# Kernel optimization log

Measured on AMD Instinct MI355X. Metric: run time of the kernel, lower is better.

The kernel has to match this reference:

```python
import jax, jax.numpy as jnp
import numpy as np
import math

EMBED_DIM = 1024
NUM_HEADS = 16
HEAD_DIM = EMBED_DIM // NUM_HEADS
ROPE_BASE = 10000.0


def setup_inputs() -> dict:
    key = jax.random.key(0)
    ks = jax.random.split(key, 11)
    B, S, E = 2, 2048, EMBED_DIM
    s = 1.0 / math.sqrt(E)
    return {
        "query": jax.random.normal(ks[0], (B, S, E), jnp.float32),
        "key": jax.random.normal(ks[1], (B, S, E), jnp.float32),
        "value": jax.random.normal(ks[2], (B, S, E), jnp.float32),
        "Wq": jax.random.normal(ks[3], (E, E), jnp.float32) * s,
        "bq": jnp.zeros((E,), jnp.float32),
        "Wk": jax.random.normal(ks[4], (E, E), jnp.float32) * s,
        "bk": jnp.zeros((E,), jnp.float32),
        "Wv": jax.random.normal(ks[5], (E, E), jnp.float32) * s,
        "bv": jnp.zeros((E,), jnp.float32),
        "Wo": jax.random.normal(ks[6], (E, E), jnp.float32) * s,
        "bo": jnp.zeros((E,), jnp.float32),
    }


def _rope_cache(S, D, dtype):
    inv_freq = 1.0 / (ROPE_BASE ** (jnp.arange(0, D, 2, dtype=jnp.float32) / D))
    t = jnp.arange(S, dtype=jnp.float32)
    freqs = t[:, None] * inv_freq[None, :]  # [S, D/2]
    return jnp.cos(freqs).astype(dtype), jnp.sin(freqs).astype(dtype)


def _apply_rope(x, cos, sin):
    # x: [B, H, S, D]; cos/sin: [S, D/2]
    x_even = x[..., 0::2]
    x_odd = x[..., 1::2]
    rot_even = x_even * cos - x_odd * sin
    rot_odd = x_odd * cos + x_even * sin
    # interleave back: [..., D/2, 2] -> [..., D]
    return jnp.stack([rot_even, rot_odd], axis=-1).reshape(x.shape)


def reference(query, key, value, Wq, bq, Wk, bk, Wv, bv, Wo, bo):
    B, S, E = query.shape
    H, D = NUM_HEADS, HEAD_DIM
    q = (query @ Wq.T + bq).reshape(B, S, H, D).transpose(0, 2, 1, 3)
    k = (key @ Wk.T + bk).reshape(B, S, H, D).transpose(0, 2, 1, 3)
    v = (value @ Wv.T + bv).reshape(B, S, H, D).transpose(0, 2, 1, 3)
    cos, sin = _rope_cache(S, D, q.dtype)
    q = _apply_rope(q, cos, sin)
    k = _apply_rope(k, cos, sin)
    scores = jnp.einsum('bhsd,bhtd->bhst', q, k) / math.sqrt(D)
    attn = jax.nn.softmax(scores, axis=-1)
    out = jnp.einsum('bhst,bhtd->bhsd', attn, v)
    out = out.transpose(0, 2, 1, 3).reshape(B, S, E)
    return out @ Wo.T + bo
```

## Files before the change

### kernel.cpp

```cpp
#include <hip/hip_runtime.h>
#include <math.h>

typedef unsigned short u16;
typedef __bf16 bf16x8 __attribute__((ext_vector_type(8)));
typedef float floatx4 __attribute__((ext_vector_type(4)));
typedef float floatx16 __attribute__((ext_vector_type(16)));

#define MFMA16(a, b, c) __builtin_amdgcn_mfma_f32_16x16x32_bf16((a), (b), (c), 0, 0, 0)
#define MFMA32(a, b, c) __builtin_amdgcn_mfma_f32_32x32x16_bf16((a), (b), (c), 0, 0, 0)

__device__ __forceinline__ float bf2f(u16 u) {
  union { float f; unsigned int i; } v; v.i = ((unsigned int)u) << 16; return v.f;
}
__device__ __forceinline__ u16 f2bf(float f) {
  __bf16 h = (__bf16)f;
  union { __bf16 h; u16 u; } v; v.h = h; return v.u;
}
__device__ __forceinline__ bf16x8 cvt8(float4 a, float4 b) {
  bf16x8 r;
  r[0] = (__bf16)a.x; r[1] = (__bf16)a.y; r[2] = (__bf16)a.z; r[3] = (__bf16)a.w;
  r[4] = (__bf16)b.x; r[5] = (__bf16)b.y; r[6] = (__bf16)b.z; r[7] = (__bf16)b.w;
  return r;
}
__device__ __forceinline__ void gl2lds16(const void* g, void* l) {
  __builtin_amdgcn_global_load_lds(
      (const __attribute__((address_space(1))) unsigned int*)g,
      (__attribute__((address_space(3))) unsigned int*)l, 16, 0, 0);
}

struct GemmArgs {
  const void* A[3];
  const float* W[3];
  const float* bias[3];
  void* C[3];
  int out_mode[3];
};

template <int BM, int ABF16>
__global__ __launch_bounds__(256) void gemm_nt(GemmArgs args) {
  const int N = 1024, K = 1024;

  const int NY = gridDim.y;
  const int lin = blockIdx.x + (blockIdx.y << 3) + blockIdx.z * (NY << 3);
  const int chunk = NY * gridDim.z;
  const int nid = (lin & 7) * chunk + (lin >> 3);
  const int z = nid / (NY << 3);
  const int rem = nid - z * (NY << 3);
  const int m0 = (rem >> 3) * BM, n0 = (rem & 7) * 128;

  const float* W = args.W[z];
  const float* bias = args.bias[z];
  const int out_mode = args.out_mode[z];
  constexpr int MI = BM / 32;

  __shared__ __align__(16) char AsB[2][ABF16 ? BM * 64 : BM * 128];
  __shared__ __align__(16) char BsB[2][128 * 128];

  const int t = threadIdx.x;
  const int wave = t >> 6, lane = t & 63;
  const int lr = lane & 15, quad = lane >> 4;
  const int wm = (wave >> 1) * (BM / 2), wn = (wave & 1) * 64;

  auto stage = [&](int kt, int bi) {
    if constexpr (ABF16) {
      const u16* Ab = (const u16*)args.A[z];
      constexpr int NI = BM / 16;
#pragma unroll
      for (int j = 0; j < (NI + 3) / 4; j++) {
        const int ii = wave + j * 4;
        if (NI >= 4 || ii < NI) {
          const int r0 = ii * 16;
          const int row = r0 + (lane >> 2);
          const int cg = (lane & 3) ^ ((lane >> 2) & 3);
          gl2lds16(Ab + (size_t)(m0 + row) * K + kt + cg * 8, AsB[bi] + r0 * 64 + lane * 16);
        }
      }
    } else {
      const float* Af = (const float*)args.A[z];
#pragma unroll
      for (int j = 0; j < BM / 32; j++) {
        const int r0 = wave * (BM / 4) + j * 8;
        const int row = r0 + (lane >> 3);
        const int cg = (lane & 7) ^ ((lane >> 3) & 7);
        gl2lds16(Af + (size_t)(m0 + row) * K + kt + cg * 4, AsB[bi] + r0 * 128 + lane * 16);
      }
    }
#pragma unroll
    for (int j = 0; j < 4; j++) {
      const int r0 = wave * 32 + j * 8;
      const int row = r0 + (lane >> 3);
      const int cg = (lane & 7) ^ ((lane >> 3) & 7);
      gl2lds16(W + (size_t)(n0 + row) * K + kt + cg * 4, BsB[bi] + r0 * 128 + lane * 16);
    }
  };

  floatx4 acc[MI][4] = {};

  stage(0, 0);
  int buf = 0;
  for (int kt = 0; kt < K; kt += 32) {
    __syncthreads();
    if (kt + 32 < K) stage(kt + 32, buf ^ 1);

    bf16x8 af[MI], bf[4];
#pragma unroll
    for (int i = 0; i < MI; i++) {
      const int row = wm + i * 16 + lr;
      if constexpr (ABF16) {
        const int cp = quad ^ (row & 3);
        af[i] = *reinterpret_cast<const bf16x8*>(AsB[buf] + row * 64 + cp * 16);
      } else {
        const int e = row & 7;
        const float4 c0 = *reinterpret_cast<const float4*>(AsB[buf] + row * 128 + ((2 * quad) ^ e) * 16);
        const float4 c1 = *reinterpret_cast<const float4*>(AsB[buf] + row * 128 + ((2 * quad + 1) ^ e) * 16);
        af[i] = cvt8(c0, c1);
      }
    }
#pragma unroll
    for (int i = 0; i < 4; i++) {
      const int row = wn + i * 16 + lr;
      const int e = row & 7;
      const float4 c0 = *reinterpret_cast<const float4*>(BsB[buf] + row * 128 + ((2 * quad) ^ e) * 16);
      const float4 c1 = *reinterpret_cast<const float4*>(BsB[buf] + row * 128 + ((2 * quad + 1) ^ e) * 16);
      bf[i] = cvt8(c0, c1);
    }
#pragma unroll
    for (int mi = 0; mi < MI; mi++)
#pragma unroll
      for (int nf = 0; nf < 4; nf++)
        acc[mi][nf] = MFMA16(af[mi], bf[nf], acc[mi][nf]);
    buf ^= 1;
  }

#pragma unroll
  for (int nf = 0; nf < 4; nf++) {
    const int col = n0 + wn + nf * 16 + lr;
    const float bv = bias[col];
#pragma unroll
    for (int mi = 0; mi < MI; mi++) {
      const int row0 = m0 + wm + mi * 16 + quad * 4;
      if (out_mode == 0) {
        u16* C = (u16*)args.C[z];
#pragma unroll
        for (int r = 0; r < 4; r++)
          C[(row0 + r) * N + col] = f2bf(acc[mi][nf][r] + bv);
      } else if (out_mode == 1) {
        u16* C = (u16*)args.C[z];
        const int h = col >> 6, d = col & 63;
        const int b = row0 >> 11, s = row0 & 2047;
        ushort4 pk;
        pk.x = f2bf(acc[mi][nf][0] + bv);
        pk.y = f2bf(acc[mi][nf][1] + bv);
        pk.z = f2bf(acc[mi][nf][2] + bv);
        pk.w = f2bf(acc[mi][nf][3] + bv);
        *reinterpret_cast<ushort4*>(&C[((b * 16 + h) * 64 + d) * 2048 + s]) = pk;
      } else {
        float* C = (float*)args.C[z];
#pragma unroll
        for (int r = 0; r < 4; r++)
          C[(row0 + r) * N + col] = acc[mi][nf][r] + bv;
      }
    }
  }
}

__global__ __launch_bounds__(256) void rope_kernel(u16* Q, u16* Kb) {
  const int idx = blockIdx.x * 256 + threadIdx.x;
  const int tensor = idx >> 19;
  const int i = idx & 524287;
  u16* P = tensor ? Kb : Q;
  const int row = i >> 7;
  const int cg = i & 127;
  const int s = row & 2047;
  const int col0 = cg * 8;
  const float scale = tensor ? 1.0f : 0.18033688011112042f;
  union { uint4 u; u16 h[8]; } v;
  v.u = *reinterpret_cast<const uint4*>(&P[row * 1024 + col0]);
  const int j0 = (col0 & 63) >> 1;
#pragma unroll
  for (int p = 0; p < 4; p++) {
    const int j = j0 + p;
    const float inv = exp2f(-(float)j * (13.287712379549449f / 32.0f));
    const float f = (float)s * inv;
    float sn, cs;
    sincosf(f, &sn, &cs);
    const float e = bf2f(v.h[2 * p]), o = bf2f(v.h[2 * p + 1]);
    v.h[2 * p]     = f2bf((e * cs - o * sn) * scale);
    v.h[2 * p + 1] = f2bf((o * cs + e * sn) * scale);
  }
  *reinterpret_cast<uint4*>(&P[row * 1024 + col0]) = v.u;
}

#define MAKE_PB(pp, g, out) do {                                              \
    unsigned int wA, wB, wC, wD;                                              \
    asm("v_cvt_pk_bf16_f32 %0, %1, %2" : "=v"(wA) : "v"((pp)[(g)+0]), "v"((pp)[(g)+1])); \
    asm("v_cvt_pk_bf16_f32 %0, %1, %2" : "=v"(wB) : "v"((pp)[(g)+4]), "v"((pp)[(g)+5])); \
    asm("v_cvt_pk_bf16_f32 %0, %1, %2" : "=v"(wC) : "v"((pp)[(g)+2]), "v"((pp)[(g)+3])); \
    asm("v_cvt_pk_bf16_f32 %0, %1, %2" : "=v"(wD) : "v"((pp)[(g)+6]), "v"((pp)[(g)+7])); \
    asm("v_permlane32_swap_b32 %0, %1" : "+v"(wA), "+v"(wB));                 \
    asm("v_permlane32_swap_b32 %0, %1" : "+v"(wC), "+v"(wD));                 \
    union { unsigned int w[4]; bf16x8 v; } u_;                                \
    u_.w[0] = wA; u_.w[1] = wC; u_.w[2] = wB; u_.w[3] = wD;                   \
    (out) = u_.v;                                                             \
  } while (0)

__global__ __launch_bounds__(256, 2) void attn_kernel(const u16* Q, const u16* K,
                                                      const u16* Vt, u16* O) {
  const int lin = blockIdx.x + (blockIdx.y << 4);
  const int nid = (lin & 7) * 64 + (lin >> 3);
  const int bx = nid & 15, bh = nid >> 4;

  const int b = bh >> 4, h = bh & 15;
  const int t = threadIdx.x;
  const int warp = t >> 6, lane = t & 63;
  const int lq = lane & 31, hi = lane >> 5;

  __shared__ __align__(16) u16 Ks[2][64][64];
  __shared__ __align__(16) u16 Vs[2][64][64];

  const int q0 = bx * 128 + warp * 32;

  const u16* qp = &Q[(size_t)(b * 2048 + q0 + lq) * 1024 + h * 64 + hi * 8];
  bf16x8 qf[4];
#pragma unroll
  for (int s = 0; s < 4; s++) qf[s] = *reinterpret_cast<const bf16x8*>(&qp[s * 16]);

  const u16* kbase = &K[(size_t)b * 2048 * 1024 + h * 64];
  const u16* vbase = &Vt[(size_t)bh * 131072];

  const int srr = lane >> 3;
  const int scg = (lane & 7) ^ srr;

  auto stage = [&](int kt2, int bufi) {
#pragma unroll
    for (int j = 0; j < 2; j++) {
      const int r0 = warp * 16 + j * 8;
      const int row = r0 + srr;
      gl2lds16(kbase + (size_t)(kt2 + row) * 1024 + scg * 8, &Ks[bufi][r0][0]);
      gl2lds16(vbase + (size_t)row * 2048 + kt2 + scg * 8, &Vs[bufi][r0][0]);
    }
  };

  floatx16 o0 = {}, o1 = {};
  float m = -1.0e30f, l = 0.0f;

  stage(0, 0);
  int buf = 0;
  for (int kt = 0; kt < 2048; kt += 64) {
    __syncthreads();
    if (kt + 64 < 2048) stage(kt + 64, buf ^ 1);

    bf16x8 kf[2][4], vf[4][2];
#pragma unroll
    for (int kb = 0; kb < 2; kb++) {
      const int r = kb * 32 + lq;
#pragma unroll
      for (int s = 0; s < 4; s++)
        kf[kb][s] = *reinterpret_cast<const bf16x8*>(&Ks[buf][r][((s * 2 + hi) ^ (r & 7)) * 8]);
    }
#pragma unroll
    for (int d = 0; d < 2; d++) {
      const int r = d * 32 + lq;
#pragma unroll
      for (int ks = 0; ks < 4; ks++)
        vf[ks][d] = *reinterpret_cast<const bf16x8*>(&Vs[buf][r][((ks * 2 + hi) ^ (r & 7)) * 8]);
    }

    floatx16 p0 = {}, p1 = {};
#pragma unroll
    for (int s = 0; s < 4; s++) {
      p0 = MFMA32(kf[0][s], qf[s], p0);
      p1 = MFMA32(kf[1][s], qf[s], p1);
    }

    float mx = p0[0];
#pragma unroll
    for (int r = 1; r < 16; r++) mx = fmaxf(mx, p0[r]);
#pragma unroll
    for (int r = 0; r < 16; r++) mx = fmaxf(mx, p1[r]);
    mx = fmaxf(mx, __shfl_xor(mx, 32, 64));
    if (!__all(mx <= m + 10.0f)) {
      const float mn = fmaxf(m, mx);
      const float al = __builtin_amdgcn_exp2f(m - mn);
      m = mn;
      l *= al;
#pragma unroll
      for (int r = 0; r < 16; r++) { o0[r] *= al; o1[r] *= al; }
    }
    float sum = 0.0f;
#pragma unroll
    for (int r = 0; r < 16; r++) { p0[r] = __builtin_amdgcn_exp2f(p0[r] - m); sum += p0[r]; }
#pragma unroll
    for (int r = 0; r < 16; r++) { p1[r] = __builtin_amdgcn_exp2f(p1[r] - m); sum += p1[r]; }
    l += sum + __shfl_xor(sum, 32, 64);

    bf16x8 pb0, pb1, pb2, pb3;
    MAKE_PB(p0, 0, pb0);
    MAKE_PB(p0, 8, pb1);
    MAKE_PB(p1, 0, pb2);
    MAKE_PB(p1, 8, pb3);

    o0 = MFMA32(vf[0][0], pb0, o0);
    o1 = MFMA32(vf[0][1], pb0, o1);
    o0 = MFMA32(vf[1][0], pb1, o0);
    o1 = MFMA32(vf[1][1], pb1, o1);
    o0 = MFMA32(vf[2][0], pb2, o0);
    o1 = MFMA32(vf[2][1], pb2, o1);
    o0 = MFMA32(vf[3][0], pb3, o0);
    o1 = MFMA32(vf[3][1], pb3, o1);

    buf ^= 1;
  }

  const float rl = 1.0f / l;
  u16* op = &O[(size_t)(b * 2048 + q0 + lq) * 1024 + h * 64 + hi * 4];
#pragma unroll
  for (int rq = 0; rq < 4; rq++) {
    ushort4 s0, s1;
    s0.x = f2bf(o0[4 * rq + 0] * rl); s0.y = f2bf(o0[4 * rq + 1] * rl);
    s0.z = f2bf(o0[4 * rq + 2] * rl); s0.w = f2bf(o0[4 * rq + 3] * rl);
    s1.x = f2bf(o1[4 * rq + 0] * rl); s1.y = f2bf(o1[4 * rq + 1] * rl);
    s1.z = f2bf(o1[4 * rq + 2] * rl); s1.w = f2bf(o1[4 * rq + 3] * rl);
    *reinterpret_cast<ushort4*>(&op[rq * 8]) = s0;
    *reinterpret_cast<ushort4*>(&op[rq * 8 + 32]) = s1;
  }
}

extern "C" void kernel_launch(void* const* d_in, const int* in_sizes, int n_in,
                              void* d_out, int out_size, void* d_ws, size_t ws_size,
                              hipStream_t stream) {
  (void)in_sizes; (void)n_in; (void)out_size; (void)ws_size;
  const float* query = (const float*)d_in[0];
  const float* key   = (const float*)d_in[1];
  const float* value = (const float*)d_in[2];
  const float* Wq = (const float*)d_in[3];
  const float* bq = (const float*)d_in[4];
  const float* Wk = (const float*)d_in[5];
  const float* bk = (const float*)d_in[6];
  const float* Wv = (const float*)d_in[7];
  const float* bv = (const float*)d_in[8];
  const float* Wo = (const float*)d_in[9];
  const float* bo = (const float*)d_in[10];

  u16* Qb = (u16*)d_ws;
  u16* Kb = (u16*)d_out;
  u16* Vt = (u16*)d_out + 4194304;

  GemmArgs g1;
  g1.A[0] = query; g1.W[0] = Wq; g1.bias[0] = bq; g1.C[0] = Qb; g1.out_mode[0] = 0;
  g1.A[1] = key;   g1.W[1] = Wk; g1.bias[1] = bk; g1.C[1] = Kb; g1.out_mode[1] = 0;
  g1.A[2] = value; g1.W[2] = Wv; g1.bias[2] = bv; g1.C[2] = Vt; g1.out_mode[2] = 1;
  gemm_nt<64, 0><<<dim3(8, 64, 3), dim3(256), 0, stream>>>(g1);

  rope_kernel<<<dim3(4096), dim3(256), 0, stream>>>(Qb, Kb);

  attn_kernel<<<dim3(16, 32), dim3(256), 0, stream>>>(Qb, Kb, Vt, Qb);

  GemmArgs g2;
  for (int i = 0; i < 3; i++) {
    g2.A[i] = Qb; g2.W[i] = Wo; g2.bias[i] = bo;
    g2.C[i] = d_out; g2.out_mode[i] = 2;
  }
  gemm_nt<32, 1><<<dim3(8, 128, 1), dim3(256), 0, stream>>>(g2);
}
```

Baseline: 261.9 us.

## Pre-convert weights and activations to bf16 and enlarge GEMM tiles

Adds a conversion kernel that casts the four weight matrices and, when workspace allows, the q/k/v activations to bf16 in workspace. The GEMMs can then stage bf16 tiles directly, which halves global and LDS traffic and drops the per-iteration fp32-to-bf16 conversion. The GEMMs also drop double buffering for a single buffer with two barriers, and the tiles grow (BM 64→128 for the projections, 32→64 for the output GEMM). The cost is extra conversion passes over the inputs, loss of load/compute overlap inside the GEMM, and lower grid parallelism.

```diff
diff --git a/kernel.cpp b/kernel.cpp
--- a/kernel.cpp
+++ b/kernel.cpp
@@ -28,15 +28,25 @@
       (__attribute__((address_space(3))) unsigned int*)l, 16, 0, 0);
 }
 
+struct CvtArgs { const float* src[3]; u16* dst[3]; };
+__global__ __launch_bounds__(256) void cvt_kernel(CvtArgs a) {
+  const float* s = a.src[blockIdx.z];
+  u16* d = a.dst[blockIdx.z];
+  const int i = (blockIdx.x * 256 + threadIdx.x) * 8;
+  const float4 x = *reinterpret_cast<const float4*>(s + i);
+  const float4 y = *reinterpret_cast<const float4*>(s + i + 4);
+  *reinterpret_cast<bf16x8*>(&d[i]) = cvt8(x, y);
+}
+
 struct GemmArgs {
   const void* A[3];
-  const float* W[3];
+  const void* W[3];
   const float* bias[3];
   void* C[3];
   int out_mode[3];
 };
 
-template <int BM, int ABF16>
+template <int BM, int ABF16, int WBF16>
 __global__ __launch_bounds__(256) void gemm_nt(GemmArgs args) {
   const int N = 1024, K = 1024;
 
@@ -48,20 +58,19 @@
   const int rem = nid - z * (NY << 3);
   const int m0 = (rem >> 3) * BM, n0 = (rem & 7) * 128;
 
-  const float* W = args.W[z];
   const float* bias = args.bias[z];
   const int out_mode = args.out_mode[z];
   constexpr int MI = BM / 32;
 
-  __shared__ __align__(16) char AsB[2][ABF16 ? BM * 64 : BM * 128];
-  __shared__ __align__(16) char BsB[2][128 * 128];
+  __shared__ __align__(16) char AsB[ABF16 ? BM * 64 : BM * 128];
+  __shared__ __align__(16) char BsB[WBF16 ? 128 * 64 : 128 * 128];
 
   const int t = threadIdx.x;
   const int wave = t >> 6, lane = t & 63;
   const int lr = lane & 15, quad = lane >> 4;
   const int wm = (wave >> 1) * (BM / 2), wn = (wave & 1) * 64;
 
-  auto stage = [&](int kt, int bi) {
+  auto stage = [&](int kt) {
     if constexpr (ABF16) {
       const u16* Ab = (const u16*)args.A[z];
       constexpr int NI = BM / 16;
@@ -72,7 +81,7 @@
           const int r0 = ii * 16;
           const int row = r0 + (lane >> 2);
           const int cg = (lane & 3) ^ ((lane >> 2) & 3);
-          gl2lds16(Ab + (size_t)(m0 + row) * K + kt + cg * 8, AsB[bi] + r0 * 64 + lane * 16);
+          gl2lds16(Ab + (size_t)(m0 + row) * K + kt + cg * 8, AsB + r0 * 64 + lane * 16);
         }
       }
     } else {
@@ -82,25 +91,36 @@
         const int r0 = wave * (BM / 4) + j * 8;
         const int row = r0 + (lane >> 3);
         const int cg = (lane & 7) ^ ((lane >> 3) & 7);
-        gl2lds16(Af + (size_t)(m0 + row) * K + kt + cg * 4, AsB[bi] + r0 * 128 + lane * 16);
-      }
-    }
-#pragma unroll
-    for (int j = 0; j < 4; j++) {
-      const int r0 = wave * 32 + j * 8;
-      const int row = r0 + (lane >> 3);
-      const int cg = (lane & 7) ^ ((lane >> 3) & 7);
-      gl2lds16(W + (size_t)(n0 + row) * K + kt + cg * 4, BsB[bi] + r0 * 128 + lane * 16);
+        gl2lds16(Af + (size_t)(m0 + row) * K + kt + cg * 4, AsB + r0 * 128 + lane * 16);
+      }
+    }
+    if constexpr (WBF16) {
+      const u16* Wb = (const u16*)args.W[z];
+#pragma unroll
+      for (int j = 0; j < 2; j++) {
+        const int r0 = (wave + j * 4) * 16;
+        const int row = r0 + (lane >> 2);
+        const int cg = (lane & 3) ^ ((lane >> 2) & 3);
+        gl2lds16(Wb + (size_t)(n0 + row) * K + kt + cg * 8, BsB + r0 * 64 + lane * 16);
+      }
+    } else {
+      const float* Wf = (const float*)args.W[z];
+#pragma unroll
+      for (int j = 0; j < 4; j++) {
+        const int r0 = wave * 32 + j * 8;
+        const int row = r0 + (lane >> 3);
+        const int cg = (lane & 7) ^ ((lane >> 3) & 7);
+        gl2lds16(Wf + (size_t)(n0 + row) * K + kt + cg * 4, BsB + r0 * 128 + lane * 16);
+      }
     }
   };
 
   floatx4 acc[MI][4] = {};
 
-  stage(0, 0);
-  int buf = 0;
   for (int kt = 0; kt < K; kt += 32) {
     __syncthreads();
-    if (kt + 32 < K) stage(kt + 32, buf ^ 1);
+    stage(kt);
+    __syncthreads();
 
     bf16x8 af[MI], bf[4];
 #pragma unroll
@@ -108,28 +128,32 @@
       const int row = wm + i * 16 + lr;
       if constexpr (ABF16) {
         const int cp = quad ^ (row & 3);
-        af[i] = *reinterpret_cast<const bf16x8*>(AsB[buf] + row * 64 + cp * 16);
+        af[i] = *reinterpret_cast<const bf16x8*>(AsB + row * 64 + cp * 16);
       } else {
         const int e = row & 7;
-        const float4 c0 = *reinterpret_cast<const float4*>(AsB[buf] + row * 128 + ((2 * quad) ^ e) * 16);
-        const float4 c1 = *reinterpret_cast<const float4*>(AsB[buf] + row * 128 + ((2 * quad + 1) ^ e) * 16);
+        const float4 c0 = *reinterpret_cast<const float4*>(AsB + row * 128 + ((2 * quad) ^ e) * 16);
+        const float4 c1 = *reinterpret_cast<const float4*>(AsB + row * 128 + ((2 * quad + 1) ^ e) * 16);
         af[i] = cvt8(c0, c1);
       }
     }
 #pragma unroll
     for (int i = 0; i < 4; i++) {
       const int row = wn + i * 16 + lr;
-      const int e = row & 7;
-      const float4 c0 = *reinterpret_cast<const float4*>(BsB[buf] + row * 128 + ((2 * quad) ^ e) * 16);
-      const float4 c1 = *reinterpret_cast<const float4*>(BsB[buf] + row * 128 + ((2 * quad + 1) ^ e) * 16);
-      bf[i] = cvt8(c0, c1);
+      if constexpr (WBF16) {
+        const int cp = quad ^ (row & 3);
+        bf[i] = *reinterpret_cast<const bf16x8*>(BsB + row * 64 + cp * 16);
+      } else {
+        const int e = row & 7;
+        const float4 c0 = *reinterpret_cast<const float4*>(BsB + row * 128 + ((2 * quad) ^ e) * 16);
+        const float4 c1 = *reinterpret_cast<const float4*>(BsB + row * 128 + ((2 * quad + 1) ^ e) * 16);
+        bf[i] = cvt8(c0, c1);
+      }
     }
 #pragma unroll
     for (int mi = 0; mi < MI; mi++)
 #pragma unroll
       for (int nf = 0; nf < 4; nf++)
         acc[mi][nf] = MFMA16(af[mi], bf[nf], acc[mi][nf]);
-    buf ^= 1;
   }
 
 #pragma unroll
@@ -329,7 +353,7 @@
 extern "C" void kernel_launch(void* const* d_in, const int* in_sizes, int n_in,
                               void* d_out, int out_size, void* d_ws, size_t ws_size,
                               hipStream_t stream) {
-  (void)in_sizes; (void)n_in; (void)out_size; (void)ws_size;
+  (void)in_sizes; (void)n_in; (void)out_size;
   const float* query = (const float*)d_in[0];
   const float* key   = (const float*)d_in[1];
   const float* value = (const float*)d_in[2];
@@ -346,11 +370,51 @@
   u16* Kb = (u16*)d_out;
   u16* Vt = (u16*)d_out + 4194304;
 
+  const bool haveW = ws_size >= (size_t)(8388608 + 4 * 2097152);
+  const bool haveA = ws_size >= (size_t)(8388608 + 4 * 2097152 + 25165824);
+  u16* Wbf = (u16*)d_ws + 4194304;
+  u16* Abf = (u16*)d_ws + 4194304 + 4194304;
+
+  if (haveW) {
+    CvtArgs cw;
+    cw.src[0] = Wq; cw.dst[0] = Wbf;
+    cw.src[1] = Wk; cw.dst[1] = Wbf + 1048576;
+    cw.src[2] = Wv; cw.dst[2] = Wbf + 2097152;
+    cvt_kernel<<<dim3(512, 1, 3), dim3(256), 0, stream>>>(cw);
+    CvtArgs co;
+    co.src[0] = Wo; co.dst[0] = Wbf + 3145728;
+    co.src[1] = Wo; co.dst[1] = Wbf + 3145728;
+    co.src[2] = Wo; co.dst[2] = Wbf + 3145728;
+    cvt_kernel<<<dim3(512, 1, 1), dim3(256), 0, stream>>>(co);
+  }
+  if (haveA) {
+    CvtArgs ca;
+    ca.src[0] = query; ca.dst[0] = Abf;
+    ca.src[1] = key;   ca.dst[1] = Abf + 4194304;
+    ca.src[2] = value; ca.dst[2] = Abf + 8388608;
+    cvt_kernel<<<dim3(2048, 1, 3), dim3(256), 0, stream>>>(ca);
+  }
+
   GemmArgs g1;
-  g1.A[0] = query; g1.W[0] = Wq; g1.bias[0] = bq; g1.C[0] = Qb; g1.out_mode[0] = 0;
-  g1.A[1] = key;   g1.W[1] = Wk; g1.bias[1] = bk; g1.C[1] = Kb; g1.out_mode[1] = 0;
-  g1.A[2] = value; g1.W[2] = Wv; g1.bias[2] = bv; g1.C[2] = Vt; g1.out_mode[2] = 1;
-  gemm_nt<64, 0><<<dim3(8, 64, 3), dim3(256), 0, stream>>>(g1);
+  g1.bias[0] = bq; g1.C[0] = Qb; g1.out_mode[0] = 0;
+  g1.bias[1] = bk; g1.C[1] = Kb; g1.out_mode[1] = 0;
+  g1.bias[2] = bv; g1.C[2] = Vt; g1.out_mode[2] = 1;
+  if (haveA) {
+    g1.A[0] = Abf; g1.A[1] = Abf + 4194304; g1.A[2] = Abf + 8388608;
+  } else {
+    g1.A[0] = query; g1.A[1] = key; g1.A[2] = value;
+  }
+  if (haveW) {
+    g1.W[0] = Wbf; g1.W[1] = Wbf + 1048576; g1.W[2] = Wbf + 2097152;
+  } else {
+    g1.W[0] = Wq; g1.W[1] = Wk; g1.W[2] = Wv;
+  }
+  if (haveA && haveW)
+    gemm_nt<128, 1, 1><<<dim3(8, 32, 3), dim3(256), 0, stream>>>(g1);
+  else if (haveW)
+    gemm_nt<128, 0, 1><<<dim3(8, 32, 3), dim3(256), 0, stream>>>(g1);
+  else
+    gemm_nt<128, 0, 0><<<dim3(8, 32, 3), dim3(256), 0, stream>>>(g1);
 
   rope_kernel<<<dim3(4096), dim3(256), 0, stream>>>(Qb, Kb);
 
@@ -358,8 +422,12 @@
 
   GemmArgs g2;
   for (int i = 0; i < 3; i++) {
-    g2.A[i] = Qb; g2.W[i] = Wo; g2.bias[i] = bo;
+    g2.A[i] = Qb; g2.bias[i] = bo;
     g2.C[i] = d_out; g2.out_mode[i] = 2;
-  }
-  gemm_nt<32, 1><<<dim3(8, 128, 1), dim3(256), 0, stream>>>(g2);
-}
+    g2.W[i] = haveW ? (const void*)(Wbf + 3145728) : (const void*)Wo;
+  }
+  if (haveW)
+    gemm_nt<64, 1, 1><<<dim3(8, 64, 1), dim3(256), 0, stream>>>(g2);
+  else
+    gemm_nt<64, 1, 0><<<dim3(8, 64, 1), dim3(256), 0, stream>>>(g2);
+}
```

Result: faster. 231.1 us (-11.8%).
